# Kernel optimization log

Hardware: AMD Instinct MI355X
Metric: run time of the kernel (lower is better)

The kernel has to match this reference:

```python
import jax, jax.numpy as jnp
import numpy as np

NEG_SLOPE = 0.2

def gat_conv(x, src, dst, W, a_src, a_dst, bias, N):
    # PyG GATConv, heads=1: h = xW; e_ij = LeakyReLU(a_src.h_j + a_dst.h_i)
    h = x @ W                                   # [N, H]
    as_ = h @ a_src                             # [N]
    ad_ = h @ a_dst                             # [N]
    e = jax.nn.leaky_relu(as_[src] + ad_[dst], NEG_SLOPE)   # [E]
    m = jax.ops.segment_max(e, dst, num_segments=N)          # per-target max
    w = jnp.exp(e - m[dst])
    denom = jax.ops.segment_sum(w, dst, num_segments=N)
    alpha = w / (denom[dst] + 1e-16)                          # [E]
    out = jax.ops.segment_sum(alpha[:, None] * h[src], dst, num_segments=N)
    return out + bias


def setup_inputs() -> dict:
    key = jax.random.key(0)
    N, E, D, H, A = 20000, 320000, 256, 256, 8
    ks = jax.random.split(key, 16)
    s = lambda k, shp, fan: jax.random.normal(k, shp, jnp.float32) * (1.0 / np.sqrt(fan))
    return {
        "obs": jax.random.normal(ks[0], (N, D), jnp.float32),
        "edge_index": jax.random.randint(ks[1], (2, E), 0, N, dtype=jnp.int32),
        "W1": s(ks[2], (D, H), D), "a1_src": s(ks[3], (H,), H), "a1_dst": s(ks[4], (H,), H), "b1": jnp.zeros((H,), jnp.float32),
        "W2": s(ks[5], (H, H), H), "a2_src": s(ks[6], (H,), H), "a2_dst": s(ks[7], (H,), H), "b2": jnp.zeros((H,), jnp.float32),
        "Wm1": s(ks[8], (H, H), H), "bm1": jnp.zeros((H,), jnp.float32),
        "Wm2": s(ks[9], (H, A), H), "bm2": jnp.zeros((A,), jnp.float32),
    }


def reference(obs, edge_index, W1, a1_src, a1_dst, b1, W2, a2_src, a2_dst, b2, Wm1, bm1, Wm2, bm2):
    N = obs.shape[0]
    loops = jnp.arange(N, dtype=edge_index.dtype)
    src = jnp.concatenate([edge_index[0], loops])   # add self-loops (PyG default)
    dst = jnp.concatenate([edge_index[1], loops])
    x = jax.nn.relu(gat_conv(obs, src, dst, W1, a1_src, a1_dst, b1, N))
    x = jax.nn.relu(gat_conv(x,   src, dst, W2, a2_src, a2_dst, b2, N))
    x = jax.nn.relu(x @ Wm1 + bm1)
    return jnp.tanh(x @ Wm2 + bm2)
```

## Files before the change

kernel.cpp:

```cpp
#include <hip/hip_runtime.h>
#include <hip/hip_bf16.h>
#include <math.h>
#include <stdio.h>

typedef __attribute__((ext_vector_type(8))) short short8;
typedef __attribute__((ext_vector_type(4))) float f32x4;
typedef __attribute__((ext_vector_type(4))) unsigned short us4;
typedef __attribute__((ext_vector_type(8))) unsigned short us8;

__device__ __forceinline__ float us2f(unsigned short u) {
    return __uint_as_float(((unsigned)u) << 16);
}
__device__ __forceinline__ unsigned short f2us_rtn(float f) {
    return (unsigned short)__bfloat16_as_ushort(__float2bfloat16(f));
}

__global__ void prep_all(const float* __restrict__ Wa, const float* __restrict__ Wb,
                         const float* __restrict__ Wc, const float* __restrict__ obs,
                         unsigned short* __restrict__ TA, unsigned short* __restrict__ TB,
                         unsigned short* __restrict__ TC, unsigned short* __restrict__ obsb,
                         float* __restrict__ as1, float* __restrict__ ad1,
                         float* __restrict__ as2, float* __restrict__ ad2,
                         int* __restrict__ deg,
                         int K, int Nn, int N, int nObs8) {
    const int tot = K * Nn;
    int idx = blockIdx.x * blockDim.x + threadIdx.x;
    if (idx < 3 * tot) {
        const float* W;
        unsigned short* T;
        if (idx < tot) { W = Wa; T = TA; }
        else if (idx < 2 * tot) { W = Wb; T = TB; idx -= tot; }
        else { W = Wc; T = TC; idx -= 2 * tot; }
        const int n = idx / K, k = idx - n * K;
        T[idx] = f2us_rtn(W[(size_t)k * Nn + n]);
        return;
    }
    idx -= 3 * tot;
    if (idx < 5 * N) {
        if (idx < N) as1[idx] = 0.f;
        else if (idx < 2 * N) ad1[idx - N] = 0.f;
        else if (idx < 3 * N) as2[idx - 2 * N] = 0.f;
        else if (idx < 4 * N) ad2[idx - 3 * N] = 0.f;
        else deg[idx - 4 * N] = 0;
        return;
    }
    idx -= 5 * N;
    if (idx < nObs8) {
        const float4 a = *(const float4*)(obs + (size_t)idx * 8);
        const float4 b = *(const float4*)(obs + (size_t)idx * 8 + 4);
        const float f[8] = {a.x, a.y, a.z, a.w, b.x, b.y, b.z, b.w};
        short8 o;
#pragma unroll
        for (int e = 0; e < 8; e++) o[e] = (short)f2us_rtn(f[e]);
        *(short8*)(obsb + (size_t)idx * 8) = o;
    }
}

#define LP 72
__global__ __launch_bounds__(256) void gemm_mfma(const unsigned short* __restrict__ A,
                                                 const unsigned short* __restrict__ Bt,
                                                 const float* __restrict__ avs,
                                                 const float* __restrict__ avd,
                                                 float* __restrict__ as_,
                                                 float* __restrict__ ad_,
                                                 unsigned short* __restrict__ C,
                                                 int M, int Nn, int K) {
    __shared__ unsigned short sA[64 * LP];
    __shared__ unsigned short sB[128 * LP];
    const int tid = threadIdx.x;
    const int wave = tid >> 6, lane = tid & 63;
    const int m16 = lane & 15, quad = lane >> 4;
    const int row0 = blockIdx.x * 64, col0 = blockIdx.y * 128;
    const int wr = (wave >> 1) * 32, wc = (wave & 1) * 64;
    const int ar = tid >> 2, akc = (tid & 3) * 8;
    const int bkc = (tid & 7) * 8, bcb = tid >> 3;
    const int gr = (row0 + ar) < M ? (row0 + ar) : (M - 1);
    const unsigned short* Arow = A + (size_t)gr * K + akc;
    const unsigned short* Bcol = Bt + (size_t)(col0 + bcb) * K + bkc;

    short8 rA0, rA1, rb0, rb1, rb2, rb3;
    auto LOADT = [&](int k0) {
        rA0 = *(const short8*)(Arow + k0);
        rA1 = *(const short8*)(Arow + k0 + 32);
        rb0 = *(const short8*)(Bcol + k0);
        rb1 = *(const short8*)(Bcol + (size_t)32 * K + k0);
        rb2 = *(const short8*)(Bcol + (size_t)64 * K + k0);
        rb3 = *(const short8*)(Bcol + (size_t)96 * K + k0);
    };
    auto STORET = [&]() {
        *(short8*)&sA[ar * LP + akc]      = rA0;
        *(short8*)&sA[ar * LP + akc + 32] = rA1;
        *(short8*)&sB[bcb * LP + bkc]        = rb0;
        *(short8*)&sB[(bcb + 32) * LP + bkc] = rb1;
        *(short8*)&sB[(bcb + 64) * LP + bkc] = rb2;
        *(short8*)&sB[(bcb + 96) * LP + bkc] = rb3;
    };

    f32x4 acc[2][4] = {};
    LOADT(0);
    STORET();
    __syncthreads();
    for (int k0 = 0; k0 < K; k0 += 64) {
        const bool more = (k0 + 64) < K;
        if (more) LOADT(k0 + 64);
#pragma unroll
        for (int ks = 0; ks < 2; ks++) {
            short8 ah[2];
#pragma unroll
            for (int mi = 0; mi < 2; mi++)
                ah[mi] = *(const short8*)&sA[(wr + mi * 16 + m16) * LP + ks * 32 + quad * 8];
#pragma unroll
            for (int ni = 0; ni < 4; ni++) {
                const short8 bv = *(const short8*)&sB[(wc + ni * 16 + m16) * LP + ks * 32 + quad * 8];
#pragma unroll
                for (int mi = 0; mi < 2; mi++)
                    acc[mi][ni] = __builtin_amdgcn_mfma_f32_16x16x32_bf16(ah[mi], bv, acc[mi][ni], 0, 0, 0);
            }
        }
        __syncthreads();
        if (more) { STORET(); __syncthreads(); }
    }
    float ps[2][4] = {}, pd[2][4] = {};
#pragma unroll
    for (int mi = 0; mi < 2; mi++) {
        const int orow_base = row0 + wr + mi * 16 + quad * 4;
#pragma unroll
        for (int ni = 0; ni < 4; ni++) {
            const int ocol = col0 + wc + ni * 16 + m16;
            const float asv = avs[ocol], adv = avd[ocol];
#pragma unroll
            for (int r = 0; r < 4; r++) {
                const int orow = orow_base + r;
                if (orow < M) {
                    const float v = acc[mi][ni][r];
                    C[(size_t)orow * Nn + ocol] = f2us_rtn(v);
                    ps[mi][r] = fmaf(v, asv, ps[mi][r]);
                    pd[mi][r] = fmaf(v, adv, pd[mi][r]);
                }
            }
        }
    }
#pragma unroll
    for (int mi = 0; mi < 2; mi++)
#pragma unroll
        for (int r = 0; r < 4; r++)
#pragma unroll
            for (int off = 1; off < 16; off <<= 1) {
                ps[mi][r] += __shfl_xor(ps[mi][r], off);
                pd[mi][r] += __shfl_xor(pd[mi][r], off);
            }
    if (m16 == 0) {
#pragma unroll
        for (int mi = 0; mi < 2; mi++) {
            const int orow_base = row0 + wr + mi * 16 + quad * 4;
#pragma unroll
            for (int r = 0; r < 4; r++) {
                const int orow = orow_base + r;
                if (orow < M) {
                    atomicAdd(&as_[orow], ps[mi][r]);
                    atomicAdd(&ad_[orow], pd[mi][r]);
                }
            }
        }
    }
}

__global__ __launch_bounds__(256) void gemm_head(const unsigned short* __restrict__ A,
                                                 const unsigned short* __restrict__ Bt,
                                                 const float* __restrict__ bias1,
                                                 const float* __restrict__ W2,
                                                 const float* __restrict__ bias2,
                                                 float* __restrict__ out,
                                                 int M, int K, int Aout) {
    __shared__ unsigned short sA[64 * LP];
    __shared__ unsigned short sB[256 * LP];
    __shared__ float pLDS[2][64][8];
    const int tid = threadIdx.x;
    const int wave = tid >> 6, lane = tid & 63;
    const int m16 = lane & 15, quad = lane >> 4;
    const int row0 = blockIdx.x * 64;
    const int wr = (wave >> 1) * 32, wc = (wave & 1) * 128;
    const int ar = tid >> 2, akc = (tid & 3) * 8;
    const int bkc = (tid & 7) * 8, bcb = tid >> 3;
    const int gr = (row0 + ar) < M ? (row0 + ar) : (M - 1);
    const unsigned short* Arow = A + (size_t)gr * K + akc;
    const unsigned short* Bcol = Bt + (size_t)bcb * K + bkc;

    short8 rA0, rA1, rb[8];
    auto LOADT = [&](int k0) {
        rA0 = *(const short8*)(Arow + k0);
        rA1 = *(const short8*)(Arow + k0 + 32);
#pragma unroll
        for (int q = 0; q < 8; q++)
            rb[q] = *(const short8*)(Bcol + (size_t)(32 * q) * K + k0);
    };
    auto STORET = [&]() {
        *(short8*)&sA[ar * LP + akc]      = rA0;
        *(short8*)&sA[ar * LP + akc + 32] = rA1;
#pragma unroll
        for (int q = 0; q < 8; q++)
            *(short8*)&sB[(bcb + 32 * q) * LP + bkc] = rb[q];
    };

    f32x4 acc[2][8] = {};
    LOADT(0);
    STORET();
    __syncthreads();
    for (int k0 = 0; k0 < K; k0 += 64) {
        const bool more = (k0 + 64) < K;
        if (more) LOADT(k0 + 64);
#pragma unroll
        for (int ks = 0; ks < 2; ks++) {
            short8 ah[2];
#pragma unroll
            for (int mi = 0; mi < 2; mi++)
                ah[mi] = *(const short8*)&sA[(wr + mi * 16 + m16) * LP + ks * 32 + quad * 8];
#pragma unroll
            for (int ni = 0; ni < 8; ni++) {
                const short8 bv = *(const short8*)&sB[(wc + ni * 16 + m16) * LP + ks * 32 + quad * 8];
#pragma unroll
                for (int mi = 0; mi < 2; mi++)
                    acc[mi][ni] = __builtin_amdgcn_mfma_f32_16x16x32_bf16(ah[mi], bv, acc[mi][ni], 0, 0, 0);
            }
        }
        __syncthreads();
        if (more) { STORET(); __syncthreads(); }
    }
    float p[2][4][8] = {};
#pragma unroll
    for (int ni = 0; ni < 8; ni++) {
        const int ocol = wc + ni * 16 + m16;
        const float b1v = bias1[ocol];
        float w2[8];
#pragma unroll
        for (int a = 0; a < 8; a++) w2[a] = W2[ocol * 8 + a];
#pragma unroll
        for (int mi = 0; mi < 2; mi++)
#pragma unroll
            for (int r = 0; r < 4; r++) {
                const float v = fmaxf(acc[mi][ni][r] + b1v, 0.f);
#pragma unroll
                for (int a = 0; a < 8; a++) p[mi][r][a] = fmaf(v, w2[a], p[mi][r][a]);
            }
    }
#pragma unroll
    for (int off = 1; off < 16; off <<= 1)
#pragma unroll
        for (int mi = 0; mi < 2; mi++)
#pragma unroll
            for (int r = 0; r < 4; r++)
#pragma unroll
                for (int a = 0; a < 8; a++) p[mi][r][a] += __shfl_xor(p[mi][r][a], off);
    if (m16 == 0) {
        const int half = wc >> 7;
#pragma unroll
        for (int mi = 0; mi < 2; mi++) {
            const int lrow = wr + mi * 16 + quad * 4;
#pragma unroll
            for (int r = 0; r < 4; r++)
#pragma unroll
                for (int a = 0; a < 8; a++) pLDS[half][lrow + r][a] = p[mi][r][a];
        }
    }
    __syncthreads();
#pragma unroll
    for (int u = 0; u < 2; u++) {
        const int idx = tid * 2 + u;
        const int lrow = idx >> 3, a = idx & 7;
        const int orow = row0 + lrow;
        if (orow < M && a < Aout)
            out[(size_t)orow * Aout + a] =
                tanhf(pLDS[0][lrow][a] + pLDS[1][lrow][a] + bias2[a]);
    }
}
#undef LP

__global__ void count_kernel(const int* __restrict__ dstA, int* __restrict__ deg, int E, int Etot) {
    const int e = blockIdx.x * blockDim.x + threadIdx.x;
    if (e >= Etot) return;
    const int d = (e < E) ? dstA[e] : (e - E);
    atomicAdd(&deg[d], 1);
}

__global__ __launch_bounds__(1024) void scan_kernel(const int* __restrict__ deg,
                                                    int* __restrict__ offs,
                                                    int* __restrict__ cursor, int N) {
    __shared__ int sums[1024];
    const int t = threadIdx.x;
    const int chunk = (N + 1023) / 1024;
    const int start = t * chunk;
    int s = 0;
    for (int i = 0; i < chunk; i++) {
        const int p = start + i;
        if (p < N) s += deg[p];
    }
    sums[t] = s;
    __syncthreads();
    for (int off = 1; off < 1024; off <<= 1) {
        const int add = (t >= off) ? sums[t - off] : 0;
        __syncthreads();
        sums[t] += add;
        __syncthreads();
    }
    int run = (t > 0) ? sums[t - 1] : 0;
    for (int i = 0; i < chunk; i++) {
        const int p = start + i;
        if (p < N) { offs[p] = run; cursor[p] = run; run += deg[p]; }
    }
    if (t == 0) offs[N] = sums[1023];
}

__global__ void scatter_kernel(const int* __restrict__ srcA, const int* __restrict__ dstA,
                               int* __restrict__ cursor, int* __restrict__ esrc, int E, int Etot) {
    const int e = blockIdx.x * blockDim.x + threadIdx.x;
    if (e >= Etot) return;
    int s, d;
    if (e < E) { s = srcA[e]; d = dstA[e]; } else { s = d = e - E; }
    const int slot = atomicAdd(&cursor[d], 1);
    esrc[slot] = s;
}

__global__ __launch_bounds__(256) void agg_kernel(const unsigned short* __restrict__ hb,
                                                  const int* __restrict__ offs,
                                                  const int* __restrict__ esrc,
                                                  const float* __restrict__ as_,
                                                  const float* __restrict__ ad_,
                                                  const float* __restrict__ bias,
                                                  unsigned short* __restrict__ xout, int N) {
    const int n = __builtin_amdgcn_readfirstlane(blockIdx.x * 4 + (threadIdx.x >> 6));
    if (n >= N) return;
    const int lane = threadIdx.x & 63;
    const int half = lane >> 5;
    const int f0 = (lane & 31) * 8;
    const int b = offs[n], e2 = offs[n + 1];
    const float adn = ad_[n];
    float a[8] = {};
    float wsum = 0.f;
    for (int c0 = b; c0 < e2; c0 += 16) {
        int s = 0;
        float w = 0.f;
        if (lane < 16) {
            const int j = c0 + lane;
            const int jj = j < e2 ? j : e2 - 1;
            s = esrc[jj];
            if (j < e2) {
                float v = as_[s] + adn;
                v = v > 0.f ? v : 0.2f * v;
                w = __expf(v);
                wsum += w;
            }
        }
        us8 pv[8];
        float wb[8];
#pragma unroll
        for (int u = 0; u < 8; u++) {
            const int el = 2 * u + half;
            const int su = __shfl(s, el);
            wb[u] = __shfl(w, el);
            pv[u] = *(const us8*)(hb + (unsigned)((su << 8) + f0));
        }
#pragma unroll
        for (int u = 0; u < 8; u++)
#pragma unroll
            for (int j2 = 0; j2 < 8; j2++)
                a[j2] = fmaf(wb[u], us2f(pv[u][j2]), a[j2]);
    }
#pragma unroll
    for (int j2 = 0; j2 < 8; j2++) a[j2] += __shfl_xor(a[j2], 32);
#pragma unroll
    for (int off = 32; off; off >>= 1) wsum += __shfl_xor(wsum, off);
    const float inv = 1.0f / (wsum + 1e-16f);
    if (half == 0) {
        const float4 b0 = *(const float4*)(bias + f0);
        const float4 b1 = *(const float4*)(bias + f0 + 4);
        const float bb[8] = {b0.x, b0.y, b0.z, b0.w, b1.x, b1.y, b1.z, b1.w};
        us8 o;
#pragma unroll
        for (int j2 = 0; j2 < 8; j2++)
            o[j2] = f2us_rtn(fmaxf(a[j2] * inv + bb[j2], 0.f));
        *(us8*)(xout + (unsigned)((n << 8) + f0)) = o;
    }
}

extern "C" void kernel_launch(void* const* d_in, const int* in_sizes, int n_in,
                              void* d_out, int out_size, void* d_ws, size_t ws_size,
                              hipStream_t stream) {
    const float* obs = (const float*)d_in[0];
    const int* eidx  = (const int*)d_in[1];
    const float* W1  = (const float*)d_in[2];
    const float* a1s = (const float*)d_in[3];
    const float* a1d = (const float*)d_in[4];
    const float* b1  = (const float*)d_in[5];
    const float* W2  = (const float*)d_in[6];
    const float* a2s = (const float*)d_in[7];
    const float* a2d = (const float*)d_in[8];
    const float* b2v = (const float*)d_in[9];
    const float* Wm1 = (const float*)d_in[10];
    const float* bm1 = (const float*)d_in[11];
    const float* Wm2 = (const float*)d_in[12];
    const float* bm2 = (const float*)d_in[13];
    float* out = (float*)d_out;

    const int Hh = in_sizes[3];
    const int Dd = in_sizes[2] / Hh;
    const int N  = in_sizes[0] / Dd;
    const int E  = in_sizes[1] / 2;
    const int Etot = E + N;
    const int Aout = in_sizes[12] / Hh;

    const int* srcA = eidx;
    const int* dstA = eidx + E;

    size_t off = 0;
    char* ws = (char*)d_ws;
    auto alloc = [&](size_t bytes) -> char* {
        char* p = ws + off;
        off = (off + bytes + 15) & ~(size_t)15;
        return p;
    };
    unsigned short* h    = (unsigned short*)alloc((size_t)N * Hh * 2);
    unsigned short* xb   = (unsigned short*)alloc((size_t)N * Hh * 2);
    unsigned short* obsb = (unsigned short*)alloc((size_t)N * Dd * 2);
    float* as1   = (float*)alloc((size_t)N * 4);
    float* ad1   = (float*)alloc((size_t)N * 4);
    float* as2   = (float*)alloc((size_t)N * 4);
    float* ad2   = (float*)alloc((size_t)N * 4);
    int* deg     = (int*)alloc((size_t)N * 4);
    int* offs    = (int*)alloc((size_t)(N + 1) * 4);
    int* cursor  = (int*)alloc((size_t)N * 4);
    int* esrc    = (int*)alloc((size_t)Etot * 4);
    const size_t wsz = (size_t)Dd * Hh;
    unsigned short* W1t = (unsigned short*)alloc(wsz * 2);
    unsigned short* W2t = (unsigned short*)alloc(wsz * 2);
    unsigned short* Wmt = (unsigned short*)alloc(wsz * 2);

    const int eb = 256;
    const int eg = (Etot + eb - 1) / eb;
    const dim3 ggrid((N + 63) / 64, Hh / 128);
    const int nrow = (N + 63) / 64;
    const int nb4 = (N + 3) / 4;
    const int nObs8 = N * Dd / 8;

    const int ptot = 3 * (int)wsz + 5 * N + nObs8;
    prep_all<<<(ptot + 255) / 256, 256, 0, stream>>>(
        W1, W2, Wm1, obs, W1t, W2t, Wmt, obsb, as1, ad1, as2, ad2, deg, Dd, Hh, N, nObs8);

    count_kernel<<<eg, eb, 0, stream>>>(dstA, deg, E, Etot);
    scan_kernel<<<1, 1024, 0, stream>>>(deg, offs, cursor, N);
    scatter_kernel<<<eg, eb, 0, stream>>>(srcA, dstA, cursor, esrc, E, Etot);

    gemm_mfma<<<ggrid, 256, 0, stream>>>(obsb, W1t, a1s, a1d, as1, ad1, h, N, Hh, Dd);
    agg_kernel<<<nb4, 256, 0, stream>>>(h, offs, esrc, as1, ad1, b1, xb, N);

    gemm_mfma<<<ggrid, 256, 0, stream>>>(xb, W2t, a2s, a2d, as2, ad2, h, N, Hh, Hh);
    agg_kernel<<<nb4, 256, 0, stream>>>(h, offs, esrc, as2, ad2, b2v, xb, N);

    gemm_head<<<nrow, 256, 0, stream>>>(xb, Wmt, bm1, Wm2, bm2, out, N, Hh, Aout);
}
```

Measured before the change: 261.7 us.

## Fuse degree count and last-block scan into first GEMM launch

The first GEMM, the degree-count atomics and the CSR prefix scan now run in one launch. Blocks beyond the GEMM tiles count in-degrees, and the last block to finish (found via an atomic done counter) runs a 256-thread vectorized scan over a padded degree array. This removes two kernel launches and the serial single-block scan, and lets the counting overlap with the GEMM. The cost is a tail where one block scans alone after every other block finishes, plus reliance on a threadfence-based last-block pattern.

```diff
diff --git a/kernel.cpp b/kernel.cpp
--- a/kernel.cpp
+++ b/kernel.cpp
@@ -1,11 +1,9 @@
 #include <hip/hip_runtime.h>
 #include <hip/hip_bf16.h>
 #include <math.h>
-#include <stdio.h>
 
 typedef __attribute__((ext_vector_type(8))) short short8;
 typedef __attribute__((ext_vector_type(4))) float f32x4;
-typedef __attribute__((ext_vector_type(4))) unsigned short us4;
 typedef __attribute__((ext_vector_type(8))) unsigned short us8;
 
 __device__ __forceinline__ float us2f(unsigned short u) {
@@ -15,16 +13,17 @@
     return (unsigned short)__bfloat16_as_ushort(__float2bfloat16(f));
 }
 
-__global__ void prep_all(const float* __restrict__ Wa, const float* __restrict__ Wb,
-                         const float* __restrict__ Wc, const float* __restrict__ obs,
-                         unsigned short* __restrict__ TA, unsigned short* __restrict__ TB,
-                         unsigned short* __restrict__ TC, unsigned short* __restrict__ obsb,
-                         float* __restrict__ as1, float* __restrict__ ad1,
-                         float* __restrict__ as2, float* __restrict__ ad2,
-                         int* __restrict__ deg,
-                         int K, int Nn, int N, int nObs8) {
+__global__ void prep_zero(const float* __restrict__ Wa, const float* __restrict__ Wb,
+                          const float* __restrict__ Wc, const float* __restrict__ obs,
+                          unsigned short* __restrict__ TA, unsigned short* __restrict__ TB,
+                          unsigned short* __restrict__ TC, unsigned short* __restrict__ obsb,
+                          float* __restrict__ as1, float* __restrict__ ad1,
+                          float* __restrict__ as2, float* __restrict__ ad2,
+                          int* __restrict__ deg, int* __restrict__ done,
+                          int K, int Nn, int N, int Npad, int nObs8) {
     const int tot = K * Nn;
     int idx = blockIdx.x * blockDim.x + threadIdx.x;
+    if (idx == 0) *done = 0;
     if (idx < 3 * tot) {
         const float* W;
         unsigned short* T;
@@ -36,15 +35,16 @@
         return;
     }
     idx -= 3 * tot;
-    if (idx < 5 * N) {
+    if (idx < 4 * N) {
         if (idx < N) as1[idx] = 0.f;
         else if (idx < 2 * N) ad1[idx - N] = 0.f;
         else if (idx < 3 * N) as2[idx - 2 * N] = 0.f;
-        else if (idx < 4 * N) ad2[idx - 3 * N] = 0.f;
-        else deg[idx - 4 * N] = 0;
+        else ad2[idx - 3 * N] = 0.f;
         return;
     }
-    idx -= 5 * N;
+    idx -= 4 * N;
+    if (idx < Npad) { deg[idx] = 0; return; }
+    idx -= Npad;
     if (idx < nObs8) {
         const float4 a = *(const float4*)(obs + (size_t)idx * 8);
         const float4 b = *(const float4*)(obs + (size_t)idx * 8 + 4);
@@ -57,20 +57,18 @@
 }
 
 #define LP 72
-__global__ __launch_bounds__(256) void gemm_mfma(const unsigned short* __restrict__ A,
-                                                 const unsigned short* __restrict__ Bt,
-                                                 const float* __restrict__ avs,
-                                                 const float* __restrict__ avd,
-                                                 float* __restrict__ as_,
-                                                 float* __restrict__ ad_,
-                                                 unsigned short* __restrict__ C,
-                                                 int M, int Nn, int K) {
-    __shared__ unsigned short sA[64 * LP];
-    __shared__ unsigned short sB[128 * LP];
+__device__ __forceinline__ void gemm_tile(const unsigned short* __restrict__ A,
+                                          const unsigned short* __restrict__ Bt,
+                                          const float* __restrict__ avs,
+                                          const float* __restrict__ avd,
+                                          float* __restrict__ as_,
+                                          float* __restrict__ ad_,
+                                          unsigned short* __restrict__ C,
+                                          int M, int Nn, int K, int row0, int col0,
+                                          unsigned short* sA, unsigned short* sB) {
     const int tid = threadIdx.x;
     const int wave = tid >> 6, lane = tid & 63;
     const int m16 = lane & 15, quad = lane >> 4;
-    const int row0 = blockIdx.x * 64, col0 = blockIdx.y * 128;
     const int wr = (wave >> 1) * 32, wc = (wave & 1) * 64;
     const int ar = tid >> 2, akc = (tid & 3) * 8;
     const int bkc = (tid & 7) * 8, bcb = tid >> 3;
@@ -163,6 +161,93 @@
             }
         }
     }
+}
+
+__device__ __forceinline__ void scan_body(const int* __restrict__ deg,
+                                          int* __restrict__ offs,
+                                          int* __restrict__ cursor,
+                                          int N, int per, int* sums) {
+    const int t = threadIdx.x;
+    const int base = t * per;
+    int s = 0;
+    for (int i = 0; i < per; i += 4) {
+        const int4 v = *(const int4*)(deg + base + i);
+        s += v.x + v.y + v.z + v.w;
+    }
+    sums[t] = s;
+    __syncthreads();
+    for (int off = 1; off < 256; off <<= 1) {
+        const int add = (t >= off) ? sums[t - off] : 0;
+        __syncthreads();
+        sums[t] += add;
+        __syncthreads();
+    }
+    int run = (t > 0) ? sums[t - 1] : 0;
+    for (int i = 0; i < per; i += 4) {
+        const int4 v = *(const int4*)(deg + base + i);
+        const int p = base + i;
+        const int vv[4] = {v.x, v.y, v.z, v.w};
+#pragma unroll
+        for (int j = 0; j < 4; j++) {
+            if (p + j < N) { offs[p + j] = run; cursor[p + j] = run; }
+            run += vv[j];
+        }
+    }
+    if (t == 255) offs[N] = run;
+}
+
+__global__ __launch_bounds__(256) void fused_cg(const unsigned short* __restrict__ A,
+                                                const unsigned short* __restrict__ Bt,
+                                                const float* __restrict__ avs,
+                                                const float* __restrict__ avd,
+                                                float* __restrict__ as_,
+                                                float* __restrict__ ad_,
+                                                unsigned short* __restrict__ C,
+                                                int M, int Nn, int K, int ntiles,
+                                                const int* __restrict__ dstA,
+                                                int* __restrict__ deg, int E, int Etot,
+                                                int* __restrict__ offs,
+                                                int* __restrict__ cursor,
+                                                int* __restrict__ done, int N, int per) {
+    __shared__ unsigned short sA[64 * LP];
+    __shared__ unsigned short sB[128 * LP];
+    __shared__ int sums[256];
+    __shared__ int slast;
+    const int tid = threadIdx.x, bid = blockIdx.x;
+    if (bid < ntiles) {
+        gemm_tile(A, Bt, avs, avd, as_, ad_, C, M, Nn, K,
+                  (bid >> 1) * 64, (bid & 1) * 128, sA, sB);
+    } else {
+        const int e = (bid - ntiles) * 256 + tid;
+        if (e < Etot) {
+            const int d = (e < E) ? dstA[e] : (e - E);
+            atomicAdd(&deg[d], 1);
+        }
+    }
+    __syncthreads();
+    if (tid == 0) {
+        __threadfence();
+        slast = (atomicAdd(done, 1) == (int)gridDim.x - 1);
+    }
+    __syncthreads();
+    if (slast) {
+        __threadfence();
+        scan_body(deg, offs, cursor, N, per, sums);
+    }
+}
+
+__global__ __launch_bounds__(256) void gemm_mfma(const unsigned short* __restrict__ A,
+                                                 const unsigned short* __restrict__ Bt,
+                                                 const float* __restrict__ avs,
+                                                 const float* __restrict__ avd,
+                                                 float* __restrict__ as_,
+                                                 float* __restrict__ ad_,
+                                                 unsigned short* __restrict__ C,
+                                                 int M, int Nn, int K) {
+    __shared__ unsigned short sA[64 * LP];
+    __shared__ unsigned short sB[128 * LP];
+    gemm_tile(A, Bt, avs, avd, as_, ad_, C, M, Nn, K,
+              blockIdx.x * 64, blockIdx.y * 128, sA, sB);
 }
 
 __global__ __launch_bounds__(256) void gemm_head(const unsigned short* __restrict__ A,
@@ -274,41 +359,6 @@
     }
 }
 #undef LP
-
-__global__ void count_kernel(const int* __restrict__ dstA, int* __restrict__ deg, int E, int Etot) {
-    const int e = blockIdx.x * blockDim.x + threadIdx.x;
-    if (e >= Etot) return;
-    const int d = (e < E) ? dstA[e] : (e - E);
-    atomicAdd(&deg[d], 1);
-}
-
-__global__ __launch_bounds__(1024) void scan_kernel(const int* __restrict__ deg,
-                                                    int* __restrict__ offs,
-                                                    int* __restrict__ cursor, int N) {
-    __shared__ int sums[1024];
-    const int t = threadIdx.x;
-    const int chunk = (N + 1023) / 1024;
-    const int start = t * chunk;
-    int s = 0;
-    for (int i = 0; i < chunk; i++) {
-        const int p = start + i;
-        if (p < N) s += deg[p];
-    }
-    sums[t] = s;
-    __syncthreads();
-    for (int off = 1; off < 1024; off <<= 1) {
-        const int add = (t >= off) ? sums[t - off] : 0;
-        __syncthreads();
-        sums[t] += add;
-        __syncthreads();
-    }
-    int run = (t > 0) ? sums[t - 1] : 0;
-    for (int i = 0; i < chunk; i++) {
-        const int p = start + i;
-        if (p < N) { offs[p] = run; cursor[p] = run; run += deg[p]; }
-    }
-    if (t == 0) offs[N] = sums[1023];
-}
 
 __global__ void scatter_kernel(const int* __restrict__ srcA, const int* __restrict__ dstA,
                                int* __restrict__ cursor, int* __restrict__ esrc, int E, int Etot) {
@@ -411,6 +461,10 @@
     const int* srcA = eidx;
     const int* dstA = eidx + E;
 
+    int per = (N + 255) / 256;
+    per = (per + 3) & ~3;
+    const int Npad = 256 * per;
+
     size_t off = 0;
     char* ws = (char*)d_ws;
     auto alloc = [&](size_t bytes) -> char* {
@@ -425,10 +479,11 @@
     float* ad1   = (float*)alloc((size_t)N * 4);
     float* as2   = (float*)alloc((size_t)N * 4);
     float* ad2   = (float*)alloc((size_t)N * 4);
-    int* deg     = (int*)alloc((size_t)N * 4);
+    int* deg     = (int*)alloc((size_t)Npad * 4);
     int* offs    = (int*)alloc((size_t)(N + 1) * 4);
     int* cursor  = (int*)alloc((size_t)N * 4);
     int* esrc    = (int*)alloc((size_t)Etot * 4);
+    int* done    = (int*)alloc(16);
     const size_t wsz = (size_t)Dd * Hh;
     unsigned short* W1t = (unsigned short*)alloc(wsz * 2);
     unsigned short* W2t = (unsigned short*)alloc(wsz * 2);
@@ -436,23 +491,27 @@
 
     const int eb = 256;
     const int eg = (Etot + eb - 1) / eb;
-    const dim3 ggrid((N + 63) / 64, Hh / 128);
     const int nrow = (N + 63) / 64;
+    const int ntiles = nrow * (Hh / 128);
+    const dim3 ggrid(nrow, Hh / 128);
     const int nb4 = (N + 3) / 4;
     const int nObs8 = N * Dd / 8;
 
-    const int ptot = 3 * (int)wsz + 5 * N + nObs8;
-    prep_all<<<(ptot + 255) / 256, 256, 0, stream>>>(
-        W1, W2, Wm1, obs, W1t, W2t, Wmt, obsb, as1, ad1, as2, ad2, deg, Dd, Hh, N, nObs8);
-
-    count_kernel<<<eg, eb, 0, stream>>>(dstA, deg, E, Etot);
-    scan_kernel<<<1, 1024, 0, stream>>>(deg, offs, cursor, N);
+    const int ptot = 3 * (int)wsz + 4 * N + Npad + nObs8;
+    prep_zero<<<(ptot + 255) / 256, 256, 0, stream>>>(
+        W1, W2, Wm1, obs, W1t, W2t, Wmt, obsb, as1, ad1, as2, ad2, deg, done,
+        Dd, Hh, N, Npad, nObs8);
+
+    fused_cg<<<ntiles + eg, 256, 0, stream>>>(
+        obsb, W1t, a1s, a1d, as1, ad1, h, N, Hh, Dd, ntiles,
+        dstA, deg, E, Etot, offs, cursor, done, N, per);
+
     scatter_kernel<<<eg, eb, 0, stream>>>(srcA, dstA, cursor, esrc, E, Etot);
 
-    gemm_mfma<<<ggrid, 256, 0, stream>>>(obsb, W1t, a1s, a1d, as1, ad1, h, N, Hh, Dd);
     agg_kernel<<<nb4, 256, 0, stream>>>(h, offs, esrc, as1, ad1, b1, xb, N);
 
     gemm_mfma<<<ggrid, 256, 0, stream>>>(xb, W2t, a2s, a2d, as2, ad2, h, N, Hh, Hh);
+
     agg_kernel<<<nb4, 256, 0, stream>>>(h, offs, esrc, as2, ad2, b2v, xb, N);
 
     gemm_head<<<nrow, 256, 0, stream>>>(xb, Wmt, bm1, Wm2, bm2, out, N, Hh, Aout);
```

Measured after the change: 298.0 us. +13.9%, slower.
